# Kernel tuning notes

Measured on AMD Instinct MI355X. Metric: run time of the kernel, lower is better.

## Reference

```python
import jax, jax.numpy as jnp
import numpy as np


def setup_inputs() -> dict:
    key = jax.random.key(0)
    k1, k2, k3, k4, k5, k6 = jax.random.split(key, 6)
    B, C, H, W = 32, 512, 56, 56
    KD = 768
    x = jax.random.normal(k1, (B, C, H, W), dtype=jnp.float32)
    keyword = jax.random.normal(k2, (B, KD), dtype=jnp.float32)
    # Conv2d(2, 1, kernel_size=7): torch kaiming-uniform-ish init scale
    fan_in_conv = 2 * 7 * 7
    bnd_c = 1.0 / np.sqrt(fan_in_conv)
    conv_w = jax.random.uniform(k3, (1, 2, 7, 7), jnp.float32, -bnd_c, bnd_c)  # OIHW
    conv_b = jax.random.uniform(k4, (1,), jnp.float32, -bnd_c, bnd_c)
    # Linear(KD, 1)
    bnd_l = 1.0 / np.sqrt(KD)
    proj_w = jax.random.uniform(k5, (1, KD), jnp.float32, -bnd_l, bnd_l)
    proj_b = jax.random.uniform(k6, (1,), jnp.float32, -bnd_l, bnd_l)
    return {"x": x, "keyword": keyword, "conv_w": conv_w, "conv_b": conv_b,
            "proj_w": proj_w, "proj_b": proj_b}


def reference(x, keyword, conv_w, conv_b, proj_w, proj_b):
    # channel-wise max+mean pool -> [B, 2, H, W]
    x_compress = jnp.concatenate(
        [jnp.max(x, axis=1, keepdims=True), jnp.mean(x, axis=1, keepdims=True)],
        axis=1)
    # 7x7 conv, 2->1 channels, SAME padding (pad=3)
    attention = jax.lax.conv_general_dilated(
        x_compress, conv_w, window_strides=(1, 1), padding=[(3, 3), (3, 3)],
        dimension_numbers=("NCHW", "OIHW", "NCHW"))
    attention = attention + conv_b[None, :, None, None]  # [B,1,H,W]
    # keyword bias: Linear(KD->1), broadcast over H,W
    keyword_bias = keyword @ proj_w.T + proj_b  # [B,1]
    attention = attention + keyword_bias[:, :, None, None]
    scale = jax.nn.sigmoid(attention)
    return x * scale
```

## Files before the change

kernel.cpp:

```cpp
#include <hip/hip_runtime.h>
#include <math.h>

#define B 32
#define C 512
#define H 56
#define W 56
#define HW (H * W)
#define HW4 (HW / 4)
#define KD 768

#define BAND 4
#define NBAND (H / BAND)
#define CG 64
#define NCG (C / CG)
#define HROWS (BAND + 6)
#define HCOLS (W + 6)

typedef float floatx4 __attribute__((ext_vector_type(4)));

__global__ __launch_bounds__(512) void pool_kernel(
    const float* __restrict__ x, float* __restrict__ cmax, float* __restrict__ cmean) {
    const int tid = threadIdx.x;
    const int pos = tid & 31;
    const int cg  = tid >> 5;
    const int p   = blockIdx.x * 32 + pos;
    const int b   = p / HW4;
    const int hw4 = p - b * HW4;

    const floatx4* xb = (const floatx4*)x + (size_t)b * C * HW4 + hw4;

    floatx4 mx = { -INFINITY, -INFINITY, -INFINITY, -INFINITY };
    floatx4 sm = { 0.f, 0.f, 0.f, 0.f };
    const int c0 = cg * 32;
    #pragma unroll 4
    for (int c = c0; c < c0 + 32; ++c) {
        floatx4 v = xb[(size_t)c * HW4];
        mx.x = fmaxf(mx.x, v.x); mx.y = fmaxf(mx.y, v.y);
        mx.z = fmaxf(mx.z, v.z); mx.w = fmaxf(mx.w, v.w);
        sm += v;
    }

    __shared__ floatx4 smax[16][32];
    __shared__ floatx4 ssum[16][32];
    smax[cg][pos] = mx;
    ssum[cg][pos] = sm;
    __syncthreads();

    if (tid < 32) {
        mx = smax[0][tid];
        sm = ssum[0][tid];
        #pragma unroll
        for (int g = 1; g < 16; ++g) {
            floatx4 m2 = smax[g][tid];
            mx.x = fmaxf(mx.x, m2.x); mx.y = fmaxf(mx.y, m2.y);
            mx.z = fmaxf(mx.z, m2.z); mx.w = fmaxf(mx.w, m2.w);
            sm += ssum[g][tid];
        }
        const float inv = 1.0f / (float)C;
        floatx4 mn = sm * inv;
        const int pp = blockIdx.x * 32 + tid;
        ((floatx4*)cmax)[pp]  = mx;
        ((floatx4*)cmean)[pp] = mn;
    }
}

__global__ __launch_bounds__(256) void fused_kernel(
    const float* __restrict__ cmax, const float* __restrict__ cmean,
    const float* __restrict__ conv_w, const float* __restrict__ conv_b,
    const float* __restrict__ keyword, const float* __restrict__ proj_w,
    const float* __restrict__ proj_b,
    const floatx4* __restrict__ x4, floatx4* __restrict__ out4) {
    __shared__ float sm[2][HROWS][HCOLS];
    __shared__ float s_w[98];
    __shared__ __align__(16) float s_scale[BAND * W];
    __shared__ float s_red[4];

    const int tid  = threadIdx.x;
    const int bid  = blockIdx.x;
    const int cg   = bid & (NCG - 1);
    const int rest = bid >> 3;
    const int band = rest % NBAND;
    const int b    = rest / NBAND;
    const int row0 = band * BAND;

    if (tid < 98) s_w[tid] = conv_w[tid];

    float part = keyword[b * KD + tid]       * proj_w[tid]
               + keyword[b * KD + tid + 256] * proj_w[tid + 256]
               + keyword[b * KD + tid + 512] * proj_w[tid + 512];
    #pragma unroll
    for (int off = 32; off > 0; off >>= 1)
        part += __shfl_down(part, off);
    if ((tid & 63) == 0) s_red[tid >> 6] = part;

    for (int idx = tid; idx < 2 * HROWS * HCOLS; idx += 256) {
        const int m   = idx / (HROWS * HCOLS);
        const int rem = idx - m * (HROWS * HCOLS);
        const int r   = rem / HCOLS;
        const int j   = rem - r * HCOLS;
        const int ih  = row0 - 3 + r;
        const int iw  = j - 3;
        float v = 0.f;
        if (ih >= 0 && ih < H && iw >= 0 && iw < W)
            v = (m == 0 ? cmax : cmean)[b * HW + ih * W + iw];
        sm[m][r][j] = v;
    }
    __syncthreads();

    if (tid < BAND * W) {
        const int dr  = tid / W;
        const int col = tid - dr * W;
        float acc = s_red[0] + s_red[1] + s_red[2] + s_red[3]
                  + proj_b[0] + conv_b[0];
        #pragma unroll
        for (int kh = 0; kh < 7; ++kh) {
            #pragma unroll
            for (int kw = 0; kw < 7; ++kw) {
                acc = fmaf(sm[0][dr + kh][col + kw], s_w[kh * 7 + kw],
                      fmaf(sm[1][dr + kh][col + kw], s_w[49 + kh * 7 + kw], acc));
            }
        }
        s_scale[tid] = 1.0f / (1.0f + __expf(-acc));
    }
    __syncthreads();

    const floatx4* s4 = (const floatx4*)s_scale;
    const size_t base = (size_t)(b * C + cg * CG) * HW4 + band * (BAND * W / 4);
    #pragma unroll 2
    for (int i = tid; i < CG * (BAND * W / 4); i += 256) {
        const int cl = i / 56;
        const int f  = i - cl * 56;
        const size_t g = base + (size_t)cl * HW4 + f;
        floatx4 xv = __builtin_nontemporal_load(&x4[g]);
        floatx4 ov = xv * s4[f];
        __builtin_nontemporal_store(ov, &out4[g]);
    }
}

extern "C" void kernel_launch(void* const* d_in, const int* in_sizes, int n_in,
                              void* d_out, int out_size, void* d_ws, size_t ws_size,
                              hipStream_t stream) {
    const float* x       = (const float*)d_in[0];
    const float* keyword = (const float*)d_in[1];
    const float* conv_w  = (const float*)d_in[2];
    const float* conv_b  = (const float*)d_in[3];
    const float* proj_w  = (const float*)d_in[4];
    const float* proj_b  = (const float*)d_in[5];
    float* out = (float*)d_out;

    float* ws    = (float*)d_ws;
    float* cmax  = ws;
    float* cmean = ws + B * HW;

    pool_kernel<<<(B * HW4) / 32, 512, 0, stream>>>(x, cmax, cmean);
    fused_kernel<<<B * NBAND * NCG, 256, 0, stream>>>(
        cmax, cmean, conv_w, conv_b, keyword, proj_w, proj_b,
        (const floatx4*)x, (floatx4*)out);
}
```

Measured before the change: 383.2 us.

## Fuse channel pooling, conv gate and scaling into one banded kernel

Merges the separate pooling kernel into the gating kernel. Each block now owns one batch row-band across all channels and recomputes the channel max/mean for its band plus a 3-row halo straight from x. This removes the workspace round trip and one launch. The cost is that each input row is pooled up to 2.5 times because of the halo, the grid shrinks to 448 larger blocks, and the final scaling pass re-reads x with plain loads in the hope of cache reuse.

```diff
diff --git a/kernel.cpp b/kernel.cpp
--- a/kernel.cpp
+++ b/kernel.cpp
@@ -7,83 +7,42 @@
 #define W 56
 #define HW (H * W)
 #define HW4 (HW / 4)
+#define W4 (W / 4)
 #define KD 768
 
-#define BAND 4
-#define NBAND (H / BAND)
-#define CG 64
-#define NCG (C / CG)
-#define HROWS (BAND + 6)
-#define HCOLS (W + 6)
+#define BH 4
+#define NBAND (H / BH)
+#define HR (BH + 6)
+#define NP4 (HR * W4)
+#define GPOOL 4
+#define CPG (C / GPOOL)
+#define NITEM (NP4 * GPOOL)
 
 typedef float floatx4 __attribute__((ext_vector_type(4)));
 
-__global__ __launch_bounds__(512) void pool_kernel(
-    const float* __restrict__ x, float* __restrict__ cmax, float* __restrict__ cmean) {
-    const int tid = threadIdx.x;
-    const int pos = tid & 31;
-    const int cg  = tid >> 5;
-    const int p   = blockIdx.x * 32 + pos;
-    const int b   = p / HW4;
-    const int hw4 = p - b * HW4;
+__global__ __launch_bounds__(256) void spatial_gate_kernel(
+    const float* __restrict__ x, const float* __restrict__ keyword,
+    const float* __restrict__ conv_w, const float* __restrict__ conv_b,
+    const float* __restrict__ proj_w, const float* __restrict__ proj_b,
+    float* __restrict__ out) {
 
-    const floatx4* xb = (const floatx4*)x + (size_t)b * C * HW4 + hw4;
-
-    floatx4 mx = { -INFINITY, -INFINITY, -INFINITY, -INFINITY };
-    floatx4 sm = { 0.f, 0.f, 0.f, 0.f };
-    const int c0 = cg * 32;
-    #pragma unroll 4
-    for (int c = c0; c < c0 + 32; ++c) {
-        floatx4 v = xb[(size_t)c * HW4];
-        mx.x = fmaxf(mx.x, v.x); mx.y = fmaxf(mx.y, v.y);
-        mx.z = fmaxf(mx.z, v.z); mx.w = fmaxf(mx.w, v.w);
-        sm += v;
-    }
-
-    __shared__ floatx4 smax[16][32];
-    __shared__ floatx4 ssum[16][32];
-    smax[cg][pos] = mx;
-    ssum[cg][pos] = sm;
-    __syncthreads();
-
-    if (tid < 32) {
-        mx = smax[0][tid];
-        sm = ssum[0][tid];
-        #pragma unroll
-        for (int g = 1; g < 16; ++g) {
-            floatx4 m2 = smax[g][tid];
-            mx.x = fmaxf(mx.x, m2.x); mx.y = fmaxf(mx.y, m2.y);
-            mx.z = fmaxf(mx.z, m2.z); mx.w = fmaxf(mx.w, m2.w);
-            sm += ssum[g][tid];
-        }
-        const float inv = 1.0f / (float)C;
-        floatx4 mn = sm * inv;
-        const int pp = blockIdx.x * 32 + tid;
-        ((floatx4*)cmax)[pp]  = mx;
-        ((floatx4*)cmean)[pp] = mn;
-    }
-}
-
-__global__ __launch_bounds__(256) void fused_kernel(
-    const float* __restrict__ cmax, const float* __restrict__ cmean,
-    const float* __restrict__ conv_w, const float* __restrict__ conv_b,
-    const float* __restrict__ keyword, const float* __restrict__ proj_w,
-    const float* __restrict__ proj_b,
-    const floatx4* __restrict__ x4, floatx4* __restrict__ out4) {
-    __shared__ float sm[2][HROWS][HCOLS];
-    __shared__ float s_w[98];
-    __shared__ __align__(16) float s_scale[BAND * W];
+    __shared__ floatx4 p_max[GPOOL][NP4];
+    __shared__ floatx4 p_sum[GPOOL][NP4];
+    __shared__ float sm[2][HR][62];
+    __shared__ float s_w[100];
+    __shared__ __align__(16) float s_scale[BH * W];
     __shared__ float s_red[4];
 
     const int tid  = threadIdx.x;
-    const int bid  = blockIdx.x;
-    const int cg   = bid & (NCG - 1);
-    const int rest = bid >> 3;
-    const int band = rest % NBAND;
-    const int b    = rest / NBAND;
-    const int row0 = band * BAND;
+    const int band = blockIdx.x % NBAND;
+    const int b    = blockIdx.x / NBAND;
+    const int row0 = band * BH;
 
     if (tid < 98) s_w[tid] = conv_w[tid];
+    if (tid == 98) s_w[98] = conv_b[0];
+    if (tid == 99) s_w[99] = proj_b[0];
+
+    for (int i = tid; i < 2 * HR * 62; i += 256) ((float*)sm)[i] = 0.f;
 
     float part = keyword[b * KD + tid]       * proj_w[tid]
                + keyword[b * KD + tid + 256] * proj_w[tid + 256]
@@ -93,25 +52,57 @@
         part += __shfl_down(part, off);
     if ((tid & 63) == 0) s_red[tid >> 6] = part;
 
-    for (int idx = tid; idx < 2 * HROWS * HCOLS; idx += 256) {
-        const int m   = idx / (HROWS * HCOLS);
-        const int rem = idx - m * (HROWS * HCOLS);
-        const int r   = rem / HCOLS;
-        const int j   = rem - r * HCOLS;
-        const int ih  = row0 - 3 + r;
-        const int iw  = j - 3;
-        float v = 0.f;
-        if (ih >= 0 && ih < H && iw >= 0 && iw < W)
-            v = (m == 0 ? cmax : cmean)[b * HW + ih * W + iw];
-        sm[m][r][j] = v;
+    const floatx4* xb = (const floatx4*)x + (size_t)b * C * HW4;
+    for (int idx = tid; idx < NITEM; idx += 256) {
+        const int g    = idx / NP4;
+        const int pos4 = idx - g * NP4;
+        const int r    = pos4 / W4;
+        const int j    = pos4 - r * W4;
+        const int ih   = row0 - 3 + r;
+        if (ih < 0 || ih >= H) continue;
+        const floatx4* p = xb + (size_t)(g * CPG) * HW4 + ih * W4 + j;
+        floatx4 mx = { -INFINITY, -INFINITY, -INFINITY, -INFINITY };
+        floatx4 ac = { 0.f, 0.f, 0.f, 0.f };
+        #pragma unroll 4
+        for (int c = 0; c < CPG; ++c) {
+            floatx4 v = p[(size_t)c * HW4];
+            mx.x = fmaxf(mx.x, v.x); mx.y = fmaxf(mx.y, v.y);
+            mx.z = fmaxf(mx.z, v.z); mx.w = fmaxf(mx.w, v.w);
+            ac += v;
+        }
+        p_max[g][pos4] = mx;
+        p_sum[g][pos4] = ac;
     }
     __syncthreads();
 
-    if (tid < BAND * W) {
+    if (tid < NP4) {
+        const int r  = tid / W4;
+        const int j  = tid - r * W4;
+        const int ih = row0 - 3 + r;
+        if (ih >= 0 && ih < H) {
+            floatx4 mx = p_max[0][tid];
+            floatx4 ac = p_sum[0][tid];
+            #pragma unroll
+            for (int g = 1; g < GPOOL; ++g) {
+                floatx4 m2 = p_max[g][tid];
+                mx.x = fmaxf(mx.x, m2.x); mx.y = fmaxf(mx.y, m2.y);
+                mx.z = fmaxf(mx.z, m2.z); mx.w = fmaxf(mx.w, m2.w);
+                ac += p_sum[g][tid];
+            }
+            const floatx4 mn = ac * (1.0f / (float)C);
+            #pragma unroll
+            for (int e = 0; e < 4; ++e) {
+                sm[0][r][3 + 4 * j + e] = mx[e];
+                sm[1][r][3 + 4 * j + e] = mn[e];
+            }
+        }
+    }
+    __syncthreads();
+
+    if (tid < BH * W) {
         const int dr  = tid / W;
         const int col = tid - dr * W;
-        float acc = s_red[0] + s_red[1] + s_red[2] + s_red[3]
-                  + proj_b[0] + conv_b[0];
+        float acc = s_red[0] + s_red[1] + s_red[2] + s_red[3] + s_w[98] + s_w[99];
         #pragma unroll
         for (int kh = 0; kh < 7; ++kh) {
             #pragma unroll
@@ -124,16 +115,22 @@
     }
     __syncthreads();
 
-    const floatx4* s4 = (const floatx4*)s_scale;
-    const size_t base = (size_t)(b * C + cg * CG) * HW4 + band * (BAND * W / 4);
-    #pragma unroll 2
-    for (int i = tid; i < CG * (BAND * W / 4); i += 256) {
-        const int cl = i / 56;
-        const int f  = i - cl * 56;
-        const size_t g = base + (size_t)cl * HW4 + f;
-        floatx4 xv = __builtin_nontemporal_load(&x4[g]);
+    const floatx4* s4   = (const floatx4*)s_scale;
+    const floatx4* x4   = (const floatx4*)x;
+    floatx4*       out4 = (floatx4*)out;
+    const int base = b * C * HW4 + row0 * W4;
+    int cl = tid / 56;
+    int f  = tid - cl * 56;
+    #pragma unroll 4
+    for (int k = 0; k < (C * BH * W4) / 256; ++k) {
+        const int g = base + cl * HW4 + f;
+        floatx4 xv = x4[g];
         floatx4 ov = xv * s4[f];
         __builtin_nontemporal_store(ov, &out4[g]);
+        const int fn = f + 32;
+        const int wrap = (fn >= 56);
+        f  = wrap ? fn - 56 : fn;
+        cl = cl + 4 + wrap;
     }
 }
 
@@ -148,12 +145,6 @@
     const float* proj_b  = (const float*)d_in[5];
     float* out = (float*)d_out;
 
-    float* ws    = (float*)d_ws;
-    float* cmax  = ws;
-    float* cmean = ws + B * HW;
-
-    pool_kernel<<<(B * HW4) / 32, 512, 0, stream>>>(x, cmax, cmean);
-    fused_kernel<<<B * NBAND * NCG, 256, 0, stream>>>(
-        cmax, cmean, conv_w, conv_b, keyword, proj_w, proj_b,
-        (const floatx4*)x, (floatx4*)out);
+    spatial_gate_kernel<<<B * NBAND, 256, 0, stream>>>(
+        x, keyword, conv_w, conv_b, proj_w, proj_b, out);
 }
```

Measured after the change: 388.1 us. Within noise of the previous version (+1.3%).
